# Kernel tuning notes

Measured on AMD Instinct MI355X. Metric: run time of the kernel, lower is better.

Reference implementation:

```python
import jax, jax.numpy as jnp
import numpy as np

N = 100_000      # nodes
E = 1_600_000    # directed edges (before self-loops)
G = 128          # graphs in batch
IN = 32          # in_channels
HID = 32         # hidden_channels (per head)
HEADS = 4
SLOPE = 0.2      # GATConv leaky_relu negative_slope


def setup_inputs() -> dict:
    key = jax.random.key(0)
    ks = jax.random.split(key, 12)
    x = jax.random.normal(ks[0], (N, IN), jnp.float32)
    edge_index = jax.random.randint(ks[1], (2, E), 0, N)
    batch = jnp.sort(jax.random.randint(ks[2], (N,), 0, G))
    g = lambda k, sh: jax.random.normal(k, sh, jnp.float32) * (1.0 / np.sqrt(sh[0]))
    return {
        "x": x, "edge_index": edge_index, "batch": batch,
        # conv1: in -> heads*hid, concat
        "W1": g(ks[3], (IN, HEADS * HID)),
        "a_src1": jax.random.normal(ks[4], (HEADS, HID), jnp.float32) * 0.1,
        "a_dst1": jax.random.normal(ks[5], (HEADS, HID), jnp.float32) * 0.1,
        "b1": jnp.zeros((HEADS * HID,), jnp.float32),
        # conv2: heads*hid -> hid, heads=1, mean (concat=False)
        "W2": g(ks[6], (HEADS * HID, 1 * HID)),
        "a_src2": jax.random.normal(ks[7], (1, HID), jnp.float32) * 0.1,
        "a_dst2": jax.random.normal(ks[8], (1, HID), jnp.float32) * 0.1,
        "b2": jnp.zeros((HID,), jnp.float32),
        # classifier
        "Wc": g(ks[9], (HID, 1)),
        "bc": jnp.zeros((1,), jnp.float32),
    }


def _segment_softmax(e, seg, n):
    # e: [E', H]; softmax over edges sharing the same destination node
    m = jax.ops.segment_max(e, seg, num_segments=n)
    ex = jnp.exp(e - m[seg])
    den = jax.ops.segment_sum(ex, seg, num_segments=n)
    return ex / den[seg]


def _gat_layer(x, src, dst, W, a_src, a_dst, b, heads, ch, concat):
    n = x.shape[0]
    h = (x @ W).reshape(n, heads, ch)              # [N, H, C]
    e_src = jnp.sum(h * a_src, axis=-1)            # [N, H]
    e_dst = jnp.sum(h * a_dst, axis=-1)            # [N, H]
    e = jax.nn.leaky_relu(e_src[src] + e_dst[dst], SLOPE)   # [E', H]
    alpha = _segment_softmax(e, dst, n)            # [E', H]
    msg = h[src] * alpha[:, :, None]               # [E', H, C]
    out = jax.ops.segment_sum(msg, dst, num_segments=n)     # [N, H, C]
    out = out.reshape(n, heads * ch) if concat else out.mean(axis=1)
    return out + b


def reference(x, edge_index, batch, W1, a_src1, a_dst1, b1, W2, a_src2, a_dst2, b2, Wc, bc):
    n = x.shape[0]
    loops = jnp.arange(n, dtype=edge_index.dtype)  # GATConv add_self_loops=True
    src = jnp.concatenate([edge_index[0], loops])
    dst = jnp.concatenate([edge_index[1], loops])
    h = jax.nn.elu(_gat_layer(x, src, dst, W1, a_src1, a_dst1, b1, HEADS, HID, True))
    # dropout: eval mode -> identity
    h = jax.nn.elu(_gat_layer(h, src, dst, W2, a_src2, a_dst2, b2, 1, HID, False))
    # global_mean_pool over batch ids
    sums = jax.ops.segment_sum(h, batch, num_segments=G)
    cnt = jax.ops.segment_sum(jnp.ones((n, 1), h.dtype), batch, num_segments=G)
    pooled = sums / jnp.maximum(cnt, 1.0)
    return pooled @ Wc + bc                        # [G, 1]
```

## Files before the change

### kernel.cpp

```cpp
#include <hip/hip_runtime.h>
#include <math.h>

#define NT 100000
#define ET 1600000
#define GT 128
#define NBK 391
#define BSH 8
#define NBLK_A 256
#define CHUNK_A 6250

typedef float f4 __attribute__((ext_vector_type(4)));

__device__ __forceinline__ float lrelu(float v) { return v > 0.0f ? v : 0.2f * v; }
__device__ __forceinline__ float elu1(float v) { return v > 0.0f ? v : __expf(v) - 1.0f; }

__global__ __launch_bounds__(256) void k_histA(const int* __restrict__ dst, int* __restrict__ histA) {
  __shared__ int histL[NBK];
  int t = threadIdx.x, blk = blockIdx.x;
  for (int i = t; i < NBK; i += 256) histL[i] = 0;
  __syncthreads();
  int e0 = blk * CHUNK_A, e1 = min(ET, e0 + CHUNK_A);
  for (int e = e0 + t; e < e1; e += 256) atomicAdd(&histL[dst[e] >> BSH], 1);
  __syncthreads();
  for (int i = t; i < NBK; i += 256) histA[i * NBLK_A + blk] = histL[i];
}

__global__ __launch_bounds__(256) void k_scanB(int* __restrict__ histA, int* __restrict__ btot) {
  __shared__ int sh[256];
  int b = blockIdx.x, t = threadIdx.x;
  int v = histA[b * NBLK_A + t];
  sh[t] = v;
  __syncthreads();
  for (int off = 1; off < 256; off <<= 1) {
    int xv = (t >= off) ? sh[t - off] : 0;
    __syncthreads();
    sh[t] += xv;
    __syncthreads();
  }
  histA[b * NBLK_A + t] = sh[t] - v;
  if (t == 255) btot[b] = sh[255];
}

__global__ __launch_bounds__(512) void k_scanC(const int* __restrict__ btot, int* __restrict__ bbase) {
  __shared__ int sh[512];
  int t = threadIdx.x;
  int v = (t < NBK) ? btot[t] : 0;
  sh[t] = v;
  __syncthreads();
  for (int off = 1; off < 512; off <<= 1) {
    int xv = (t >= off) ? sh[t - off] : 0;
    __syncthreads();
    sh[t] += xv;
    __syncthreads();
  }
  if (t < NBK) bbase[t] = sh[t] - v;
  if (t == 0) bbase[NBK] = ET;
}

__global__ __launch_bounds__(256) void k_buck(const int* __restrict__ src, const int* __restrict__ dst,
                                              const int* __restrict__ histA, const int* __restrict__ bbase,
                                              unsigned int* __restrict__ ebuf) {
  __shared__ int cur[NBK];
  int t = threadIdx.x, blk = blockIdx.x;
  for (int i = t; i < NBK; i += 256) cur[i] = histA[i * NBLK_A + blk] + bbase[i];
  __syncthreads();
  int e0 = blk * CHUNK_A, e1 = min(ET, e0 + CHUNK_A);
  for (int e = e0 + t; e < e1; e += 256) {
    unsigned int s = (unsigned int)src[e];
    int d = dst[e];
    int pos = atomicAdd(&cur[d >> BSH], 1);
    ebuf[pos] = ((unsigned int)(d & 255) << 17) | s;
  }
}

__global__ __launch_bounds__(256) void k_fine(const unsigned int* __restrict__ ebuf, const int* __restrict__ bbase,
                                              int* __restrict__ rp, int* __restrict__ adj) {
  __shared__ int cnt[256];
  __shared__ int sh[256];
  __shared__ int cur[256];
  int b = blockIdx.x, t = threadIdx.x;
  int eb0 = bbase[b], eb1 = bbase[b + 1];
  cnt[t] = 0;
  __syncthreads();
  for (int e = eb0 + t; e < eb1; e += 256) atomicAdd(&cnt[ebuf[e] >> 17], 1);
  __syncthreads();
  int v = cnt[t];
  sh[t] = v;
  __syncthreads();
  for (int off = 1; off < 256; off <<= 1) {
    int xv = (t >= off) ? sh[t - off] : 0;
    __syncthreads();
    sh[t] += xv;
    __syncthreads();
  }
  int start = eb0 + sh[t] - v;
  cur[t] = start;
  int node = (b << BSH) + t;
  if (node < NT) rp[node] = start;
  if (node == NT - 1) rp[NT] = ET;
  __syncthreads();
  for (int e = eb0 + t; e < eb1; e += 256) {
    unsigned int p = ebuf[e];
    int pos = atomicAdd(&cur[p >> 17], 1);
    adj[pos] = (int)(p & 0x1FFFFu);
  }
}

__global__ void k_prep(const float* __restrict__ W1, const float* __restrict__ as1,
                       const float* __restrict__ ad1, float* __restrict__ AB) {
  int t = threadIdx.x;
  int k = t >> 3, j = t & 7;
  const float* a = (j < 4) ? as1 : ad1;
  int h = j & 3;
  float s = 0.0f;
  for (int c = 0; c < 32; ++c) s += W1[k * 128 + h * 32 + c] * a[h * 32 + c];
  AB[t] = s;
}

__global__ __launch_bounds__(256) void k_att1(const float* __restrict__ x, const float* __restrict__ AB,
                                              float* __restrict__ es, float* __restrict__ ed) {
  __shared__ float xsh[32 * 33];
  __shared__ float absh[256];
  int t = threadIdx.x;
  int n0 = blockIdx.x * 32;
  absh[t] = AB[t];
  for (int i = t; i < 1024; i += 256) {
    int ln = i >> 5, k = i & 31;
    int node = n0 + ln;
    xsh[ln * 33 + k] = (node < NT) ? x[node * 32 + k] : 0.0f;
  }
  __syncthreads();
  int ln = t >> 3, j = t & 7;
  int node = n0 + ln;
  if (node < NT) {
    float s = 0.0f;
#pragma unroll
    for (int k = 0; k < 32; ++k) s += xsh[ln * 33 + k] * absh[k * 8 + j];
    if (j < 4) es[node * 4 + j] = s;
    else ed[node * 4 + (j - 4)] = s;
  }
}

__global__ __launch_bounds__(256) void k_agg1f(
    const int* __restrict__ rp, const int* __restrict__ adj,
    const float* __restrict__ es, const float* __restrict__ ed,
    const float* __restrict__ x,
    const float* __restrict__ W1, const float* __restrict__ b1,
    const float* __restrict__ W2,
    const float* __restrict__ as2, const float* __restrict__ ad2,
    float* __restrict__ h2, float* __restrict__ es2, float* __restrict__ ed2) {
  __shared__ int sbuf[8][34];
  __shared__ f4 wbufv[8][34];
  __shared__ float ysh[8][132];
  __shared__ float osh[8][136];
  __shared__ float psh[8][33];
  int t = threadIdx.x;
  int wv = t >> 6, l = t & 63;
  int g = l >> 5, j = l & 31;
  int ns = wv * 2 + g;
  int n = blockIdx.x * 8 + ns;
  bool valid = (n < NT);
  int nc = valid ? n : NT - 1;
  const f4* es4 = (const f4*)es;
  int rs = rp[nc], re = rp[nc + 1];
  int deg = re - rs;
  f4 edn = ((const f4*)ed)[nc];
  f4 esn = es4[nc];
  float sv[4];
#pragma unroll
  for (int h = 0; h < 4; ++h) sv[h] = __expf(lrelu(esn[h] + edn[h]));
  int eg2 = j >> 3, q = j & 7;
  f4 a0 = {0,0,0,0}, a1 = {0,0,0,0}, a2 = {0,0,0,0}, a3 = {0,0,0,0};

  if (deg <= 32) {
    float ex[4] = {0.0f, 0.0f, 0.0f, 0.0f};
    if (j < deg) {
      int s = adj[rs + j];
      sbuf[ns][j] = s;
      f4 ev = es4[s];
#pragma unroll
      for (int h = 0; h < 4; ++h) ex[h] = __expf(lrelu(ev[h] + edn[h]));
    }
    float d[4] = {ex[0], ex[1], ex[2], ex[3]};
#pragma unroll
    for (int off = 1; off <= 16; off <<= 1)
#pragma unroll
      for (int h = 0; h < 4; ++h) d[h] += __shfl_xor(d[h], off);
    float inv[4];
#pragma unroll
    for (int h = 0; h < 4; ++h) inv[h] = 1.0f / (d[h] + sv[h]);
    if (j < deg) {
      f4 w4;
#pragma unroll
      for (int h = 0; h < 4; ++h) w4[h] = ex[h] * inv[h];
      wbufv[ns][j] = w4;
    }
    if (j == 0) {
      sbuf[ns][deg] = nc;
      f4 w4;
#pragma unroll
      for (int h = 0; h < 4; ++h) w4[h] = sv[h] * inv[h];
      wbufv[ns][deg] = w4;
    }
    __builtin_amdgcn_wave_barrier();
    for (int e = eg2; e <= deg; e += 4) {
      f4 xv = *(const f4*)&x[sbuf[ns][e] * 32 + 4 * q];
      f4 w4 = wbufv[ns][e];
      a0 += w4.x * xv; a1 += w4.y * xv; a2 += w4.z * xv; a3 += w4.w * xv;
    }
  } else {
    float d[4] = {0.0f, 0.0f, 0.0f, 0.0f};
    for (int jj = rs + j; jj < re; jj += 32) {
      f4 ev = es4[adj[jj]];
#pragma unroll
      for (int h = 0; h < 4; ++h) d[h] += __expf(lrelu(ev[h] + edn[h]));
    }
#pragma unroll
    for (int off = 1; off <= 16; off <<= 1)
#pragma unroll
      for (int h = 0; h < 4; ++h) d[h] += __shfl_xor(d[h], off);
    float inv[4];
#pragma unroll
    for (int h = 0; h < 4; ++h) inv[h] = 1.0f / (d[h] + sv[h]);
    for (int base = rs; base < re; base += 32) {
      int cnt = min(32, re - base);
      if (j < cnt) {
        int s = adj[base + j];
        sbuf[ns][j] = s;
        f4 ev = es4[s];
        f4 w4;
#pragma unroll
        for (int h = 0; h < 4; ++h) w4[h] = __expf(lrelu(ev[h] + edn[h])) * inv[h];
        wbufv[ns][j] = w4;
      }
      __builtin_amdgcn_wave_barrier();
      for (int e = eg2; e < cnt; e += 4) {
        f4 xv = *(const f4*)&x[sbuf[ns][e] * 32 + 4 * q];
        f4 w4 = wbufv[ns][e];
        a0 += w4.x * xv; a1 += w4.y * xv; a2 += w4.z * xv; a3 += w4.w * xv;
      }
      __builtin_amdgcn_wave_barrier();
    }
    if (eg2 == 0) {
      f4 xv = *(const f4*)&x[nc * 32 + 4 * q];
      a0 += sv[0] * inv[0] * xv; a1 += sv[1] * inv[1] * xv;
      a2 += sv[2] * inv[2] * xv; a3 += sv[3] * inv[3] * xv;
    }
  }

#pragma unroll
  for (int off = 8; off <= 16; off <<= 1) {
#pragma unroll
    for (int cc = 0; cc < 4; ++cc) {
      a0[cc] += __shfl_xor(a0[cc], off);
      a1[cc] += __shfl_xor(a1[cc], off);
      a2[cc] += __shfl_xor(a2[cc], off);
      a3[cc] += __shfl_xor(a3[cc], off);
    }
  }
  if (eg2 == 0) {
    *(f4*)&ysh[ns][0 * 33 + 4 * q] = a0;
    *(f4*)&ysh[ns][1 * 33 + 4 * q] = a1;
    *(f4*)&ysh[ns][2 * 33 + 4 * q] = a2;
    *(f4*)&ysh[ns][3 * 33 + 4 * q] = a3;
  }
  __syncthreads();

  {
    int kh = t & 1, c1 = t >> 1;
    int h1 = c1 >> 5;
    float o[8];
#pragma unroll
    for (int nd = 0; nd < 8; ++nd) o[nd] = 0.0f;
#pragma unroll
    for (int kk = 0; kk < 16; ++kk) {
      int k = kh * 16 + kk;
      float w = W1[k * 128 + c1];
      int yi = h1 * 33 + k;
#pragma unroll
      for (int nd = 0; nd < 8; ++nd) o[nd] += ysh[nd][yi] * w;
    }
#pragma unroll
    for (int nd = 0; nd < 8; ++nd) o[nd] += __shfl_xor(o[nd], 1);
    if (kh == 0) {
      float bb = b1[c1];
      int cp = c1 + (c1 >> 4);
#pragma unroll
      for (int nd = 0; nd < 8; ++nd) osh[nd][cp] = elu1(o[nd] + bb);
    }
  }
  __syncthreads();

  {
    int kg = t & 7, c2 = t >> 3;
    float p[8];
#pragma unroll
    for (int nd = 0; nd < 8; ++nd) p[nd] = 0.0f;
#pragma unroll
    for (int kk = 0; kk < 16; ++kk) {
      int k = kg * 16 + kk;
      float w = W2[k * 32 + c2];
      int kp = kg * 17 + kk;
#pragma unroll
      for (int nd = 0; nd < 8; ++nd) p[nd] += osh[nd][kp] * w;
    }
#pragma unroll
    for (int off = 1; off <= 4; off <<= 1)
#pragma unroll
      for (int nd = 0; nd < 8; ++nd) p[nd] += __shfl_xor(p[nd], off);
    if (kg == 0) {
#pragma unroll
      for (int nd = 0; nd < 8; ++nd) psh[nd][c2] = p[nd];
    }
  }
  __syncthreads();

  {
    int nd = t >> 5, j2 = t & 31;
    int n2 = blockIdx.x * 8 + nd;
    if (n2 < NT) {
      float p = psh[nd][j2];
      h2[n2 * 32 + j2] = p;
      float ps = p * as2[j2], pd = p * ad2[j2];
#pragma unroll
      for (int off = 1; off <= 16; off <<= 1) {
        ps += __shfl_xor(ps, off);
        pd += __shfl_xor(pd, off);
      }
      if (j2 == 0) { es2[n2] = ps; ed2[n2] = pd; }
    }
  }
}

__global__ __launch_bounds__(256) void k_agg2(const int* __restrict__ rp, const int* __restrict__ adj,
                                              const float* __restrict__ es, const float* __restrict__ ed,
                                              const float* __restrict__ h, const float* __restrict__ b2,
                                              const float* __restrict__ Wc, float* __restrict__ z) {
  __shared__ int sbuf[8][34];
  __shared__ float wsh[8][34];
  int t = threadIdx.x;
  int wv = t >> 6, l = t & 63;
  int g = l >> 5, j = l & 31;
  int ns = wv * 2 + g;
  int n = blockIdx.x * 8 + ns;
  if (n >= NT) return;
  int rs = rp[n], re = rp[n + 1];
  int deg = re - rs;
  float edn = ed[n];
  float sv = __expf(lrelu(es[n] + edn));
  int eg2 = j >> 3, q = j & 7;
  f4 acc = {0,0,0,0};

  if (deg <= 32) {
    float ex = 0.0f;
    if (j < deg) {
      int s = adj[rs + j];
      sbuf[ns][j] = s;
      ex = __expf(lrelu(es[s] + edn));
    }
    float d = ex;
#pragma unroll
    for (int off = 1; off <= 16; off <<= 1) d += __shfl_xor(d, off);
    float inv = 1.0f / (d + sv);
    if (j < deg) wsh[ns][j] = ex * inv;
    if (j == 0) { sbuf[ns][deg] = n; wsh[ns][deg] = sv * inv; }
    __builtin_amdgcn_wave_barrier();
    for (int e = eg2; e <= deg; e += 4) {
      acc += wsh[ns][e] * *(const f4*)&h[sbuf[ns][e] * 32 + 4 * q];
    }
  } else {
    float d = 0.0f;
    for (int jj = rs + j; jj < re; jj += 32) d += __expf(lrelu(es[adj[jj]] + edn));
#pragma unroll
    for (int off = 1; off <= 16; off <<= 1) d += __shfl_xor(d, off);
    float inv = 1.0f / (d + sv);
    for (int base = rs; base < re; base += 32) {
      int cnt = min(32, re - base);
      if (j < cnt) {
        int s = adj[base + j];
        sbuf[ns][j] = s;
        wsh[ns][j] = __expf(lrelu(es[s] + edn)) * inv;
      }
      __builtin_amdgcn_wave_barrier();
      for (int e = eg2; e < cnt; e += 4) {
        acc += wsh[ns][e] * *(const f4*)&h[sbuf[ns][e] * 32 + 4 * q];
      }
      __builtin_amdgcn_wave_barrier();
    }
    if (eg2 == 0) acc += sv * inv * *(const f4*)&h[n * 32 + 4 * q];
  }

#pragma unroll
  for (int off = 8; off <= 16; off <<= 1)
#pragma unroll
    for (int cc = 0; cc < 4; ++cc) acc[cc] += __shfl_xor(acc[cc], off);
  if (eg2 == 0) {
    f4 o = acc + *(const f4*)&b2[4 * q];
#pragma unroll
    for (int cc = 0; cc < 4; ++cc) o[cc] = elu1(o[cc]);
    f4 wc = *(const f4*)&Wc[4 * q];
    float zz = o.x * wc.x + o.y * wc.y + o.z * wc.z + o.w * wc.w;
#pragma unroll
    for (int off = 1; off <= 4; off <<= 1) zz += __shfl_xor(zz, off);
    if (q == 0) z[n] = zz;
  }
}

__global__ __launch_bounds__(256) void k_poolz(const float* __restrict__ z, const int* __restrict__ batch,
                                               const float* __restrict__ bc, float* __restrict__ out) {
  int g = blockIdx.x;
  int lo = 0, hi = NT;
  while (lo < hi) { int mid = (lo + hi) >> 1; if (batch[mid] < g) lo = mid + 1; else hi = mid; }
  int start = lo;
  hi = NT;
  while (lo < hi) { int mid = (lo + hi) >> 1; if (batch[mid] < g + 1) lo = mid + 1; else hi = mid; }
  int end = lo;

  int t = threadIdx.x;
  float s = 0.0f;
  for (int n = start + t; n < end; n += 256) s += z[n];
#pragma unroll
  for (int off = 1; off <= 32; off <<= 1) s += __shfl_xor(s, off);
  __shared__ float sh[4];
  if ((t & 63) == 0) sh[t >> 6] = s;
  __syncthreads();
  if (t == 0) {
    float tot = sh[0] + sh[1] + sh[2] + sh[3];
    float cnt = (float)(end - start);
    out[g] = tot / fmaxf(cnt, 1.0f) + bc[0];
  }
}

extern "C" void kernel_launch(void* const* d_in, const int* in_sizes, int n_in,
                              void* d_out, int out_size, void* d_ws, size_t ws_size,
                              hipStream_t stream) {
  const float* x = (const float*)d_in[0];
  const int* ei = (const int*)d_in[1];
  const int* src = ei;
  const int* dst = ei + ET;
  const int* batch = (const int*)d_in[2];
  const float* W1 = (const float*)d_in[3];
  const float* asrc1 = (const float*)d_in[4];
  const float* adst1 = (const float*)d_in[5];
  const float* b1 = (const float*)d_in[6];
  const float* W2 = (const float*)d_in[7];
  const float* asrc2 = (const float*)d_in[8];
  const float* adst2 = (const float*)d_in[9];
  const float* b2 = (const float*)d_in[10];
  const float* Wc = (const float*)d_in[11];
  const float* bc = (const float*)d_in[12];
  float* out = (float*)d_out;
  char* ws = (char*)d_ws;

  int* row_ptr = (int*)(ws + 0);
  int* histA = (int*)(ws + 400128);
  int* btot = (int*)(ws + 800512);
  int* bbase = (int*)(ws + 802112);
  float* AB = (float*)(ws + 803712);
  unsigned int* ebuf = (unsigned int*)(ws + 804736);
  int* adj = (int*)(ws + 7204736);
  float* es1 = (float*)(ws + 13604736);
  float* ed1 = (float*)(ws + 15204736);
  float* es2 = (float*)(ws + 16804736);
  float* ed2 = (float*)(ws + 17204736);
  float* h2 = (float*)(ws + 17604736);
  float* z = (float*)(ws + 30404736);

  k_histA<<<NBLK_A, 256, 0, stream>>>(dst, histA);
  k_scanB<<<NBK, 256, 0, stream>>>(histA, btot);
  k_scanC<<<1, 512, 0, stream>>>(btot, bbase);
  k_buck<<<NBLK_A, 256, 0, stream>>>(src, dst, histA, bbase, ebuf);
  k_fine<<<NBK, 256, 0, stream>>>(ebuf, bbase, row_ptr, adj);

  k_prep<<<1, 256, 0, stream>>>(W1, asrc1, adst1, AB);
  k_att1<<<(NT + 31) / 32, 256, 0, stream>>>(x, AB, es1, ed1);

  k_agg1f<<<(NT + 7) / 8, 256, 0, stream>>>(row_ptr, adj, es1, ed1, x, W1, b1, W2,
                                            asrc2, adst2, h2, es2, ed2);

  k_agg2<<<(NT + 7) / 8, 256, 0, stream>>>(row_ptr, adj, es2, ed2, h2, b2, Wc, z);

  k_poolz<<<GT, 256, 0, stream>>>(z, batch, bc, out);
}
```

Before: 228.0 us.

## Split aggregation from dense transforms into separate kernel with shared-memory weights

The fused layer-1 aggregation kernel is split in two. The first kernel writes the per-head aggregated input features y (N×128) to global memory. A new kernel then processes 32 nodes per block, with W1 and a transposed W2 staged in shared memory, and runs the W1 projection, ELU, W2 projection and layer-2 attention scores. This removes the per-block global weight reads and block-wide syncs from the gather-bound kernel and gives the dense math better reuse. The cost is an extra launch and a write and read of a 51 MB intermediate, plus 68 KB of shared memory per block in the new kernel, which limits its occupancy.

Result: slower. 242.8 us (+6.5%).

```diff
diff --git a/kernel.cpp b/kernel.cpp
--- a/kernel.cpp
+++ b/kernel.cpp
@@ -141,19 +141,12 @@
   }
 }
 
-__global__ __launch_bounds__(256) void k_agg1f(
+__global__ __launch_bounds__(256) void k_agg1g(
     const int* __restrict__ rp, const int* __restrict__ adj,
     const float* __restrict__ es, const float* __restrict__ ed,
-    const float* __restrict__ x,
-    const float* __restrict__ W1, const float* __restrict__ b1,
-    const float* __restrict__ W2,
-    const float* __restrict__ as2, const float* __restrict__ ad2,
-    float* __restrict__ h2, float* __restrict__ es2, float* __restrict__ ed2) {
+    const float* __restrict__ x, float* __restrict__ y) {
   __shared__ int sbuf[8][34];
   __shared__ f4 wbufv[8][34];
-  __shared__ float ysh[8][132];
-  __shared__ float osh[8][136];
-  __shared__ float psh[8][33];
   int t = threadIdx.x;
   int wv = t >> 6, l = t & 63;
   int g = l >> 5, j = l & 31;
@@ -258,77 +251,77 @@
       a3[cc] += __shfl_xor(a3[cc], off);
     }
   }
-  if (eg2 == 0) {
-    *(f4*)&ysh[ns][0 * 33 + 4 * q] = a0;
-    *(f4*)&ysh[ns][1 * 33 + 4 * q] = a1;
-    *(f4*)&ysh[ns][2 * 33 + 4 * q] = a2;
-    *(f4*)&ysh[ns][3 * 33 + 4 * q] = a3;
-  }
-  __syncthreads();
-
-  {
-    int kh = t & 1, c1 = t >> 1;
-    int h1 = c1 >> 5;
-    float o[8];
-#pragma unroll
-    for (int nd = 0; nd < 8; ++nd) o[nd] = 0.0f;
-#pragma unroll
-    for (int kk = 0; kk < 16; ++kk) {
-      int k = kh * 16 + kk;
-      float w = W1[k * 128 + c1];
-      int yi = h1 * 33 + k;
-#pragma unroll
-      for (int nd = 0; nd < 8; ++nd) o[nd] += ysh[nd][yi] * w;
-    }
-#pragma unroll
-    for (int nd = 0; nd < 8; ++nd) o[nd] += __shfl_xor(o[nd], 1);
-    if (kh == 0) {
-      float bb = b1[c1];
-      int cp = c1 + (c1 >> 4);
-#pragma unroll
-      for (int nd = 0; nd < 8; ++nd) osh[nd][cp] = elu1(o[nd] + bb);
-    }
-  }
-  __syncthreads();
-
-  {
-    int kg = t & 7, c2 = t >> 3;
-    float p[8];
-#pragma unroll
-    for (int nd = 0; nd < 8; ++nd) p[nd] = 0.0f;
-#pragma unroll
-    for (int kk = 0; kk < 16; ++kk) {
-      int k = kg * 16 + kk;
-      float w = W2[k * 32 + c2];
-      int kp = kg * 17 + kk;
-#pragma unroll
-      for (int nd = 0; nd < 8; ++nd) p[nd] += osh[nd][kp] * w;
-    }
-#pragma unroll
-    for (int off = 1; off <= 4; off <<= 1)
-#pragma unroll
-      for (int nd = 0; nd < 8; ++nd) p[nd] += __shfl_xor(p[nd], off);
-    if (kg == 0) {
-#pragma unroll
-      for (int nd = 0; nd < 8; ++nd) psh[nd][c2] = p[nd];
-    }
-  }
-  __syncthreads();
-
-  {
-    int nd = t >> 5, j2 = t & 31;
-    int n2 = blockIdx.x * 8 + nd;
-    if (n2 < NT) {
-      float p = psh[nd][j2];
-      h2[n2 * 32 + j2] = p;
-      float ps = p * as2[j2], pd = p * ad2[j2];
-#pragma unroll
-      for (int off = 1; off <= 16; off <<= 1) {
-        ps += __shfl_xor(ps, off);
-        pd += __shfl_xor(pd, off);
-      }
-      if (j2 == 0) { es2[n2] = ps; ed2[n2] = pd; }
-    }
+  if (eg2 == 0 && valid) {
+    *(f4*)&y[n * 128 + 0 * 32 + 4 * q] = a0;
+    *(f4*)&y[n * 128 + 1 * 32 + 4 * q] = a1;
+    *(f4*)&y[n * 128 + 2 * 32 + 4 * q] = a2;
+    *(f4*)&y[n * 128 + 3 * 32 + 4 * q] = a3;
+  }
+}
+
+__global__ __launch_bounds__(256) void k_mv(
+    const float* __restrict__ y,
+    const float* __restrict__ W1, const float* __restrict__ b1,
+    const float* __restrict__ W2,
+    const float* __restrict__ as2, const float* __restrict__ ad2,
+    float* __restrict__ h2, float* __restrict__ es2, float* __restrict__ ed2) {
+  __shared__ float W1sh[4096];
+  __shared__ float W2t[32 * 132];
+  __shared__ float b1sh[128];
+  __shared__ float ysh[32][132];
+  __shared__ float osh[32][132];
+  int t = threadIdx.x;
+  int n0 = blockIdx.x * 32;
+  for (int i = t; i < 4096; i += 256) {
+    float w = W1[i];
+    W1sh[i] = w;
+    float w2 = W2[i];
+    int k = i >> 5, c = i & 31;
+    W2t[c * 132 + k] = w2;
+  }
+  if (t < 128) b1sh[t] = b1[t];
+  for (int i = t; i < 4096; i += 256) {
+    int nd = i >> 7, c = i & 127;
+    int node = n0 + nd;
+    ysh[nd][(c >> 5) * 33 + (c & 31)] = (node < NT) ? y[node * 128 + c] : 0.0f;
+  }
+  __syncthreads();
+
+  int j2 = t & 31, grp = t >> 5;
+  int h = j2 >> 3;
+  float as2v = as2[j2], ad2v = ad2[j2];
+#pragma unroll
+  for (int i = 0; i < 4; ++i) {
+    int nd = grp * 4 + i;
+    int node = n0 + nd;
+    f4 o = {0, 0, 0, 0};
+#pragma unroll
+    for (int k = 0; k < 32; ++k) {
+      o += ysh[nd][h * 33 + k] * *(const f4*)&W1sh[k * 128 + 4 * j2];
+    }
+    o += *(const f4*)&b1sh[4 * j2];
+#pragma unroll
+    for (int cc = 0; cc < 4; ++cc) o[cc] = elu1(o[cc]);
+    *(f4*)&osh[nd][4 * j2] = o;
+    __builtin_amdgcn_wave_barrier();
+    float p = 0.0f;
+#pragma unroll
+    for (int k4 = 0; k4 < 128; k4 += 4) {
+      f4 ov = *(const f4*)&osh[nd][k4];
+      f4 wv = *(const f4*)&W2t[j2 * 132 + k4];
+      p += ov.x * wv.x + ov.y * wv.y + ov.z * wv.z + ov.w * wv.w;
+    }
+    float ps = p * as2v, pd = p * ad2v;
+#pragma unroll
+    for (int off = 1; off <= 16; off <<= 1) {
+      ps += __shfl_xor(ps, off);
+      pd += __shfl_xor(pd, off);
+    }
+    if (node < NT) {
+      h2[node * 32 + j2] = p;
+      if (j2 == 0) { es2[node] = ps; ed2[node] = pd; }
+    }
+    __builtin_amdgcn_wave_barrier();
   }
 }
 
@@ -465,6 +458,7 @@
   float* ed2 = (float*)(ws + 17204736);
   float* h2 = (float*)(ws + 17604736);
   float* z = (float*)(ws + 30404736);
+  float* y = (float*)(ws + 30804736);
 
   k_histA<<<NBLK_A, 256, 0, stream>>>(dst, histA);
   k_scanB<<<NBK, 256, 0, stream>>>(histA, btot);
@@ -475,8 +469,9 @@
   k_prep<<<1, 256, 0, stream>>>(W1, asrc1, adst1, AB);
   k_att1<<<(NT + 31) / 32, 256, 0, stream>>>(x, AB, es1, ed1);
 
-  k_agg1f<<<(NT + 7) / 8, 256, 0, stream>>>(row_ptr, adj, es1, ed1, x, W1, b1, W2,
-                                            asrc2, adst2, h2, es2, ed2);
+  k_agg1g<<<(NT + 7) / 8, 256, 0, stream>>>(row_ptr, adj, es1, ed1, x, y);
+
+  k_mv<<<(NT + 31) / 32, 256, 0, stream>>>(y, W1, b1, W2, asrc2, adst2, h2, es2, ed2);
 
   k_agg2<<<(NT + 7) / 8, 256, 0, stream>>>(row_ptr, adj, es2, ed2, h2, b2, Wc, z);
 
```
